# Optimization experiments

Hardware: AMD Instinct MI355X
Metric: run time of the kernel (lower is better)

The kernel has to match this reference:

```python
import jax, jax.numpy as jnp
import numpy as np

N_HEADS = 16
D_EMBED = 1024
D_CROSS = 768
D_HEAD = D_EMBED // N_HEADS
B, S = 4, 2048


def setup_inputs() -> dict:
    key = jax.random.key(0)
    ks = jax.random.split(key, 10)
    sq = lambda k, shp, fan: jax.random.normal(k, shp, jnp.float32) / np.sqrt(fan)
    return {
        "x": jax.random.normal(ks[0], (B, S, D_EMBED), jnp.float32),
        "y": jax.random.normal(ks[1], (B, S, D_CROSS), jnp.float32),
        "Wq": sq(ks[2], (D_EMBED, D_EMBED), D_EMBED),
        "bq": jnp.zeros((D_EMBED,), jnp.float32),
        "Wk": sq(ks[3], (D_CROSS, D_EMBED), D_CROSS),
        "bk": jnp.zeros((D_EMBED,), jnp.float32),
        "Wv": sq(ks[4], (D_CROSS, D_EMBED), D_CROSS),
        "bv": jnp.zeros((D_EMBED,), jnp.float32),
        "Wo": sq(ks[5], (D_EMBED, D_EMBED), D_EMBED),
        "bo": jnp.zeros((D_EMBED,), jnp.float32),
    }


def reference(x, y, Wq, bq, Wk, bk, Wv, bv, Wo, bo):
    b, s, _ = y.shape
    q = x @ Wq + bq  # [b, s, d_embed]
    k = y @ Wk + bk
    v = y @ Wv + bv
    # [b, h, s, d_head]
    q = q.reshape(b, s, N_HEADS, D_HEAD).transpose(0, 2, 1, 3)
    k = k.reshape(b, s, N_HEADS, D_HEAD).transpose(0, 2, 1, 3)
    v = v.reshape(b, s, N_HEADS, D_HEAD).transpose(0, 2, 1, 3)
    scale = 1.0 / np.sqrt(D_HEAD).astype(np.float32)
    scores = jnp.einsum("bhqd,bhkd->bhqk", q, k) * scale
    weights = jax.nn.softmax(scores, axis=-1)
    out = jnp.einsum("bhqk,bhkd->bhqd", weights, v)
    out = out.transpose(0, 2, 1, 3).reshape(x.shape)
    return out @ Wo + bo
```

## Files before the change

### kernel.cpp

```cpp
#include <hip/hip_runtime.h>

#define NHEADS 16
#define DEMBED 1024
#define DCROSS 768
#define DHEAD  64
#define BATCH  4
#define SLEN   2048
#define MROWS  (BATCH * SLEN)

using bf16   = __bf16;
using bf16x8 = __attribute__((ext_vector_type(8))) __bf16;
using bf16x4 = __attribute__((ext_vector_type(4))) __bf16;
using f32x4  = __attribute__((ext_vector_type(4))) float;

__device__ __forceinline__ f32x4 mfma_bf16(bf16x8 a, bf16x8 b, f32x4 c) {
    return __builtin_amdgcn_mfma_f32_16x16x32_bf16(a, b, c, 0, 0, 0);
}

__device__ __forceinline__ void gl2lds16(const void* g, void* l) {
    __builtin_amdgcn_global_load_lds(
        (const __attribute__((address_space(1))) void*)g,
        (__attribute__((address_space(3))) void*)l, 16, 0, 0);
}

struct PrepArgs {
    const float* wsrc[4]; bf16* wdst[4]; int wK[4];
    const float *x, *y; bf16 *xb, *yb;
};
#define NTRB 4096
__global__ void prep_all(PrepArgs a) {
    const int bid = blockIdx.x;
    const int tid = threadIdx.x;
    if (bid < NTRB) {
        __shared__ float tile[32][33];
        const int which = bid >> 10, rem = bid & 1023;
        const int K = a.wK[which], N = DEMBED;
        const int n0 = (rem & 31) * 32, k0 = (rem >> 5) * 32;
        if (k0 >= K) return;
        const float* W = a.wsrc[which];
        bf16* Wt = a.wdst[which];
        const int tx = tid & 31, ty = tid >> 5;
#pragma unroll
        for (int i = 0; i < 32; i += 8)
            tile[ty + i][tx] = W[(size_t)(k0 + ty + i) * N + n0 + tx];
        __syncthreads();
#pragma unroll
        for (int i = 0; i < 32; i += 8)
            Wt[(size_t)(n0 + ty + i) * K + k0 + tx] = (bf16)tile[tx][ty + i];
    } else {
        const int n4x = MROWS * DEMBED / 4;
        const int n4y = MROWS * DCROSS / 4;
        int i = (bid - NTRB) * 256 + tid;
        const float* src; bf16* dst; int j;
        if (i < n4x) { src = a.x; dst = a.xb; j = i; }
        else { j = i - n4x; if (j >= n4y) return; src = a.y; dst = a.yb; }
        float4 v = ((const float4*)src)[j];
        bf16x4 o = { (bf16)v.x, (bf16)v.y, (bf16)v.z, (bf16)v.w };
        ((bf16x4*)dst)[j] = o;
    }
}

struct QkvArgs {
    const bf16 *xb, *yb, *Wqt, *Wkt, *Wvt;
    const float *bq, *bk, *bv;
    bf16 *Qb, *Kb, *Vt;
    float qscale;
};
__global__ __launch_bounds__(256, 3) void gemm_qkv(QkvArgs a) {
    __shared__ bf16 As[128 * 64];
    __shared__ bf16 Bs[128 * 64];
    const int id = blockIdx.x;
    const int cls = id >> 9;
    const bf16 *A, *Bt;
    const float* bias;
    int K, m0, n0;
    if (cls == 0) { int t = id;        m0 = (t >> 3) * 128; n0 = (t & 7) * 128;
                    A = a.xb;  Bt = a.Wqt; bias = a.bq; K = DEMBED; }
    else if (cls == 1) { int t = id - 512;  m0 = (t >> 3) * 128; n0 = (t & 7) * 128;
                    A = a.yb;  Bt = a.Wkt; bias = a.bk; K = DCROSS; }
    else { int t = id - 1024; m0 = (t >> 6) * 128; n0 = (t & 63) * 128;
                    A = a.Wvt; Bt = a.yb;  bias = a.bv; K = DCROSS; }

    const int tid  = threadIdx.x;
    const int wave = tid >> 6, lane = tid & 63;
    const int quad = lane >> 4, l15 = lane & 15;
    const int wr = wave >> 1, wc = wave & 1;

    const int srow = wave * 8 + (lane >> 3);
    const int scol = ((lane & 7) ^ (lane >> 3)) * 8;
    char* ldsA0 = (char*)As + wave * 1024;
    char* ldsB0 = (char*)Bs + wave * 1024;
    const bf16* gA0 = A + (size_t)(m0 + srow) * K + scol;
    const bf16* gB0 = Bt + (size_t)(n0 + srow) * K + scol;

    const int sw = l15 & 7;

    f32x4 acc[4][4] = {};

    for (int kt = 0; kt < K; kt += 64) {
        __syncthreads();
#pragma unroll
        for (int c = 0; c < 4; c++)
            gl2lds16(gA0 + (size_t)c * 32 * K + kt, ldsA0 + c * 4096);
#pragma unroll
        for (int c = 0; c < 4; c++)
            gl2lds16(gB0 + (size_t)c * 32 * K + kt, ldsB0 + c * 4096);
        __syncthreads();

#pragma unroll
        for (int kg = 0; kg < 2; kg++) {
            bf16x8 af[4], bfr[4];
#pragma unroll
            for (int i = 0; i < 4; i++)
                af[i] = *(const bf16x8*)((const char*)As +
                         (wr * 64 + i * 16 + l15) * 128 + (((kg * 4 + quad) ^ sw) * 16));
#pragma unroll
            for (int i = 0; i < 4; i++)
                bfr[i] = *(const bf16x8*)((const char*)Bs +
                         (wc * 64 + i * 16 + l15) * 128 + (((kg * 4 + quad) ^ sw) * 16));
#pragma unroll
            for (int fr = 0; fr < 4; fr++)
#pragma unroll
                for (int fc = 0; fc < 4; fc++)
                    acc[fr][fc] = mfma_bf16(af[fr], bfr[fc], acc[fr][fc]);
        }
    }

    if (cls < 2) {
        bf16* Cout = (cls == 0) ? a.Qb : a.Kb;
        const float alpha = (cls == 0) ? a.qscale : 1.0f;
#pragma unroll
        for (int fr = 0; fr < 4; fr++) {
            int row = m0 + wr * 64 + fr * 16 + quad * 4;
#pragma unroll
            for (int fc = 0; fc < 4; fc++) {
                int col = n0 + wc * 64 + fc * 16 + l15;
                float bv = bias[col];
#pragma unroll
                for (int r = 0; r < 4; r++)
                    Cout[(size_t)(row + r) * DEMBED + col] =
                        (bf16)((acc[fr][fc][r] + bv) * alpha);
            }
        }
    } else {
        const int b = n0 >> 11;
        const size_t bbase = (size_t)b * DEMBED * SLEN;
#pragma unroll
        for (int fr = 0; fr < 4; fr++) {
            int row = m0 + wr * 64 + fr * 16 + quad * 4;
#pragma unroll
            for (int fc = 0; fc < 4; fc++) {
                int col = n0 + wc * 64 + fc * 16 + l15;
                int s = col & (SLEN - 1);
#pragma unroll
                for (int r = 0; r < 4; r++)
                    a.Vt[bbase + (size_t)(row + r) * SLEN + s] =
                        (bf16)(acc[fr][fc][r] + bias[row + r]);
            }
        }
    }
}

__global__ __launch_bounds__(256, 3) void gemm_o(const bf16* __restrict__ A,
                                                 const bf16* __restrict__ Bt,
                                                 const float* __restrict__ bias,
                                                 float* __restrict__ Cout) {
    const int K = DEMBED, N = DEMBED;
    __shared__ bf16 As[128 * 64];
    __shared__ bf16 Bs[128 * 64];
    const int tid  = threadIdx.x;
    const int wave = tid >> 6, lane = tid & 63;
    const int quad = lane >> 4, l15 = lane & 15;
    const int m0 = blockIdx.x * 128, n0 = blockIdx.y * 128;
    const int wr = wave >> 1, wc = wave & 1;

    const int srow = wave * 8 + (lane >> 3);
    const int scol = ((lane & 7) ^ (lane >> 3)) * 8;
    char* ldsA0 = (char*)As + wave * 1024;
    char* ldsB0 = (char*)Bs + wave * 1024;
    const bf16* gA0 = A + (size_t)(m0 + srow) * K + scol;
    const bf16* gB0 = Bt + (size_t)(n0 + srow) * K + scol;

    const int sw = l15 & 7;

    f32x4 acc[4][4] = {};

    for (int kt = 0; kt < K; kt += 64) {
        __syncthreads();
#pragma unroll
        for (int c = 0; c < 4; c++)
            gl2lds16(gA0 + (size_t)c * 32 * K + kt, ldsA0 + c * 4096);
#pragma unroll
        for (int c = 0; c < 4; c++)
            gl2lds16(gB0 + (size_t)c * 32 * K + kt, ldsB0 + c * 4096);
        __syncthreads();

#pragma unroll
        for (int kg = 0; kg < 2; kg++) {
            bf16x8 af[4], bfr[4];
#pragma unroll
            for (int i = 0; i < 4; i++)
                af[i] = *(const bf16x8*)((const char*)As +
                         (wr * 64 + i * 16 + l15) * 128 + (((kg * 4 + quad) ^ sw) * 16));
#pragma unroll
            for (int i = 0; i < 4; i++)
                bfr[i] = *(const bf16x8*)((const char*)Bs +
                         (wc * 64 + i * 16 + l15) * 128 + (((kg * 4 + quad) ^ sw) * 16));
#pragma unroll
            for (int fr = 0; fr < 4; fr++)
#pragma unroll
                for (int fc = 0; fc < 4; fc++)
                    acc[fr][fc] = mfma_bf16(af[fr], bfr[fc], acc[fr][fc]);
        }
    }

#pragma unroll
    for (int fr = 0; fr < 4; fr++) {
        int row = m0 + wr * 64 + fr * 16 + quad * 4;
#pragma unroll
        for (int fc = 0; fc < 4; fc++) {
            int col = n0 + wc * 64 + fc * 16 + l15;
            float bv = bias[col];
#pragma unroll
            for (int r = 0; r < 4; r++)
                Cout[(size_t)(row + r) * N + col] = acc[fr][fc][r] + bv;
        }
    }
}

__global__ __launch_bounds__(256, 4) void attn(const bf16* __restrict__ Q,
                                               const bf16* __restrict__ K,
                                               const bf16* __restrict__ Vt,
                                               bf16* __restrict__ O) {
    __shared__ bf16 KsA[64 * 64];
    __shared__ bf16 VsA[64 * 64];
    __shared__ bf16 PsA[4 * 32 * 72];

    const int tid  = threadIdx.x;
    const int wave = tid >> 6, lane = tid & 63;
    const int quad = lane >> 4, l15 = lane & 15;
    const int bh = blockIdx.x, b = bh >> 4, h = bh & 15;
    const size_t rowbase = (size_t)b * SLEN;
    const int qb = blockIdx.y * 128 + wave * 32;
    const int hc = h * DHEAD;

    bf16x8 qf[2][2];
#pragma unroll
    for (int rg = 0; rg < 2; rg++)
#pragma unroll
        for (int kg = 0; kg < 2; kg++)
            qf[rg][kg] = *(const bf16x8*)(Q + (rowbase + qb + rg * 16 + l15) * DEMBED
                                          + hc + kg * 32 + quad * 8);

    f32x4 o[2][4] = {};
    f32x4 lsv[2] = {};

    const bf16* Kbase = K + rowbase * DEMBED + hc;
    const bf16* Vbase = Vt + (size_t)bh * DHEAD * SLEN;

    const int xcol = (((tid & 7) ^ ((tid >> 3) & 7)) * 8);
    const bf16* gK = Kbase + (size_t)(tid >> 3) * DEMBED + xcol;
    const bf16* gV = Vbase + (size_t)(tid >> 3) * SLEN + xcol;
    char* ldsK = (char*)KsA + wave * 1024;
    char* ldsV = (char*)VsA + wave * 1024;
    bf16* Pw = PsA + wave * (32 * 72);

    for (int kb = 0; kb < SLEN; kb += 64) {
        __syncthreads();
        gl2lds16(gK + (size_t)kb * DEMBED, ldsK);
        gl2lds16(gK + (size_t)(kb + 32) * DEMBED, ldsK + 32 * 128);
        gl2lds16(gV + kb, ldsV);
        gl2lds16(gV + 32 * SLEN + kb, ldsV + 32 * 128);
        __syncthreads();

        f32x4 s[2][4] = {};
#pragma unroll
        for (int cg = 0; cg < 4; cg++)
#pragma unroll
            for (int kg = 0; kg < 2; kg++) {
                bf16x8 kf = *(const bf16x8*)((const char*)KsA +
                            (cg * 16 + l15) * 128 + (((kg * 4 + quad) ^ (l15 & 7)) * 16));
#pragma unroll
                for (int rg = 0; rg < 2; rg++)
                    s[rg][cg] = mfma_bf16(kf, qf[rg][kg], s[rg][cg]);
            }

#pragma unroll
        for (int rg = 0; rg < 2; rg++)
#pragma unroll
            for (int cg = 0; cg < 4; cg++) {
                f32x4 p;
                p[0] = __builtin_amdgcn_exp2f(s[rg][cg][0]);
                p[1] = __builtin_amdgcn_exp2f(s[rg][cg][1]);
                p[2] = __builtin_amdgcn_exp2f(s[rg][cg][2]);
                p[3] = __builtin_amdgcn_exp2f(s[rg][cg][3]);
                lsv[rg] += p;
                bf16x4 pb = { (bf16)p[0], (bf16)p[1], (bf16)p[2], (bf16)p[3] };
                *(bf16x4*)(Pw + (rg * 16 + l15) * 72 + cg * 16 + quad * 4) = pb;
            }

#pragma unroll
        for (int dg = 0; dg < 4; dg++)
#pragma unroll
            for (int kg = 0; kg < 2; kg++) {
                bf16x8 vf = *(const bf16x8*)((const char*)VsA +
                            (dg * 16 + l15) * 128 + (((kg * 4 + quad) ^ (l15 & 7)) * 16));
#pragma unroll
                for (int rg = 0; rg < 2; rg++)
                    o[rg][dg] = mfma_bf16(
                        *(const bf16x8*)(Pw + (rg * 16 + l15) * 72 + kg * 32 + quad * 8),
                        vf, o[rg][dg]);
            }
    }

    float inv[2];
#pragma unroll
    for (int rg = 0; rg < 2; rg++) {
        float rs = lsv[rg][0] + lsv[rg][1] + lsv[rg][2] + lsv[rg][3];
        rs += __shfl_xor(rs, 16);
        rs += __shfl_xor(rs, 32);
        inv[rg] = 1.0f / rs;
    }
#pragma unroll
    for (int rg = 0; rg < 2; rg++)
#pragma unroll
        for (int r = 0; r < 4; r++) {
            float iv = __shfl(inv[rg], quad * 4 + r);
#pragma unroll
            for (int dg = 0; dg < 4; dg++)
                O[(rowbase + qb + rg * 16 + quad * 4 + r) * DEMBED + hc + dg * 16 + l15] =
                    (bf16)(o[rg][dg][r] * iv);
        }
}

extern "C" void kernel_launch(void* const* d_in, const int* in_sizes, int n_in,
                              void* d_out, int out_size, void* d_ws, size_t ws_size,
                              hipStream_t stream) {
    const float* x  = (const float*)d_in[0];
    const float* y  = (const float*)d_in[1];
    const float* Wq = (const float*)d_in[2];
    const float* bq = (const float*)d_in[3];
    const float* Wk = (const float*)d_in[4];
    const float* bk = (const float*)d_in[5];
    const float* Wv = (const float*)d_in[6];
    const float* bv = (const float*)d_in[7];
    const float* Wo = (const float*)d_in[8];
    const float* bo = (const float*)d_in[9];
    float* out = (float*)d_out;

    char* ws = (char*)d_ws;
    size_t off = 0;
    auto alloc = [&](size_t bytes) {
        void* p = ws + off;
        off += (bytes + 255) & ~(size_t)255;
        return p;
    };
    bf16* xb  = (bf16*)alloc((size_t)MROWS * DEMBED * 2);
    bf16* yb  = (bf16*)alloc((size_t)MROWS * DCROSS * 2);
    bf16* Wqt = (bf16*)alloc((size_t)DEMBED * DEMBED * 2);
    bf16* Wkt = (bf16*)alloc((size_t)DEMBED * DCROSS * 2);
    bf16* Wvt = (bf16*)alloc((size_t)DEMBED * DCROSS * 2);
    bf16* Wot = (bf16*)alloc((size_t)DEMBED * DEMBED * 2);
    bf16* Qb  = (bf16*)alloc((size_t)MROWS * DEMBED * 2);
    bf16* Kb  = (bf16*)alloc((size_t)MROWS * DEMBED * 2);
    bf16* Vtb = (bf16*)alloc((size_t)MROWS * DEMBED * 2);
    bf16* Ab  = (bf16*)alloc((size_t)MROWS * DEMBED * 2);
    if (off > ws_size) return;

    {
        PrepArgs a;
        a.wsrc[0] = Wq; a.wdst[0] = Wqt; a.wK[0] = DEMBED;
        a.wsrc[1] = Wk; a.wdst[1] = Wkt; a.wK[1] = DCROSS;
        a.wsrc[2] = Wv; a.wdst[2] = Wvt; a.wK[2] = DCROSS;
        a.wsrc[3] = Wo; a.wdst[3] = Wot; a.wK[3] = DEMBED;
        a.x = x; a.y = y; a.xb = xb; a.yb = yb;
        int ncvt = (MROWS * DEMBED / 4 + MROWS * DCROSS / 4 + 255) / 256;
        prep_all<<<NTRB + ncvt, 256, 0, stream>>>(a);
    }

    {
        QkvArgs a;
        a.xb = xb; a.yb = yb; a.Wqt = Wqt; a.Wkt = Wkt; a.Wvt = Wvt;
        a.bq = bq; a.bk = bk; a.bv = bv;
        a.Qb = Qb; a.Kb = Kb; a.Vt = Vtb;
        a.qscale = 0.125f * 1.4426950408889634f;
        gemm_qkv<<<1536, 256, 0, stream>>>(a);
    }

    attn<<<dim3(BATCH * NHEADS, SLEN / 128), 256, 0, stream>>>(Qb, Kb, Vtb, Ab);

    gemm_o<<<dim3(MROWS / 128, DEMBED / 128), 256, 0, stream>>>(Ab, Wot, bo, out);
}
```

Baseline: 286.4 us.

## Load K/V fragments directly from global in attention, doubling query rows per wave

The attention kernel no longer stages K and V tiles in shared memory with block-wide barriers. Each wave now loads its K and V MFMA fragments straight from global memory (relying on cache) and processes 64 query rows instead of 32, so every fragment feeds more MFMAs. The grid is halved to match and launch bounds drop to 2 blocks per CU to allow the larger register footprint. The risks are uncoalesced, redundant global/L2 traffic for K/V across waves and lower occupancy.

```diff
diff --git a/kernel.cpp b/kernel.cpp
--- a/kernel.cpp
+++ b/kernel.cpp
@@ -228,101 +228,88 @@
     }
 }
 
-__global__ __launch_bounds__(256, 4) void attn(const bf16* __restrict__ Q,
+__global__ __launch_bounds__(256, 2) void attn(const bf16* __restrict__ Q,
                                                const bf16* __restrict__ K,
                                                const bf16* __restrict__ Vt,
                                                bf16* __restrict__ O) {
-    __shared__ bf16 KsA[64 * 64];
-    __shared__ bf16 VsA[64 * 64];
-    __shared__ bf16 PsA[4 * 32 * 72];
+    __shared__ bf16 PsA[4 * 64 * 72];
 
     const int tid  = threadIdx.x;
     const int wave = tid >> 6, lane = tid & 63;
     const int quad = lane >> 4, l15 = lane & 15;
     const int bh = blockIdx.x, b = bh >> 4, h = bh & 15;
     const size_t rowbase = (size_t)b * SLEN;
-    const int qb = blockIdx.y * 128 + wave * 32;
+    const int qb = blockIdx.y * 256 + wave * 64;
     const int hc = h * DHEAD;
 
-    bf16x8 qf[2][2];
-#pragma unroll
-    for (int rg = 0; rg < 2; rg++)
+    bf16x8 qf[4][2];
+#pragma unroll
+    for (int rg = 0; rg < 4; rg++)
 #pragma unroll
         for (int kg = 0; kg < 2; kg++)
             qf[rg][kg] = *(const bf16x8*)(Q + (rowbase + qb + rg * 16 + l15) * DEMBED
                                           + hc + kg * 32 + quad * 8);
 
-    f32x4 o[2][4] = {};
-    f32x4 lsv[2] = {};
-
-    const bf16* Kbase = K + rowbase * DEMBED + hc;
-    const bf16* Vbase = Vt + (size_t)bh * DHEAD * SLEN;
-
-    const int xcol = (((tid & 7) ^ ((tid >> 3) & 7)) * 8);
-    const bf16* gK = Kbase + (size_t)(tid >> 3) * DEMBED + xcol;
-    const bf16* gV = Vbase + (size_t)(tid >> 3) * SLEN + xcol;
-    char* ldsK = (char*)KsA + wave * 1024;
-    char* ldsV = (char*)VsA + wave * 1024;
-    bf16* Pw = PsA + wave * (32 * 72);
+    f32x4 o[4][4] = {};
+    f32x4 lsv[4] = {};
+
+    const bf16* Kp = K + (rowbase + l15) * DEMBED + hc + quad * 8;
+    const bf16* Vp = Vt + ((size_t)bh * DHEAD + l15) * SLEN + quad * 8;
+
+    bf16* Pw = PsA + wave * (64 * 72);
 
     for (int kb = 0; kb < SLEN; kb += 64) {
-        __syncthreads();
-        gl2lds16(gK + (size_t)kb * DEMBED, ldsK);
-        gl2lds16(gK + (size_t)(kb + 32) * DEMBED, ldsK + 32 * 128);
-        gl2lds16(gV + kb, ldsV);
-        gl2lds16(gV + 32 * SLEN + kb, ldsV + 32 * 128);
-        __syncthreads();
-
-        f32x4 s[2][4] = {};
-#pragma unroll
-        for (int cg = 0; cg < 4; cg++)
-#pragma unroll
-            for (int kg = 0; kg < 2; kg++) {
-                bf16x8 kf = *(const bf16x8*)((const char*)KsA +
-                            (cg * 16 + l15) * 128 + (((kg * 4 + quad) ^ (l15 & 7)) * 16));
-#pragma unroll
-                for (int rg = 0; rg < 2; rg++)
-                    s[rg][cg] = mfma_bf16(kf, qf[rg][kg], s[rg][cg]);
-            }
-
-#pragma unroll
-        for (int rg = 0; rg < 2; rg++)
-#pragma unroll
-            for (int cg = 0; cg < 4; cg++) {
+#pragma unroll
+        for (int cg = 0; cg < 4; cg++) {
+            const bf16* kp = Kp + (size_t)(kb + cg * 16) * DEMBED;
+            bf16x8 kf0 = *(const bf16x8*)(kp);
+            bf16x8 kf1 = *(const bf16x8*)(kp + 32);
+            f32x4 s[4] = {};
+#pragma unroll
+            for (int rg = 0; rg < 4; rg++) {
+                s[rg] = mfma_bf16(kf0, qf[rg][0], s[rg]);
+                s[rg] = mfma_bf16(kf1, qf[rg][1], s[rg]);
+            }
+#pragma unroll
+            for (int rg = 0; rg < 4; rg++) {
                 f32x4 p;
-                p[0] = __builtin_amdgcn_exp2f(s[rg][cg][0]);
-                p[1] = __builtin_amdgcn_exp2f(s[rg][cg][1]);
-                p[2] = __builtin_amdgcn_exp2f(s[rg][cg][2]);
-                p[3] = __builtin_amdgcn_exp2f(s[rg][cg][3]);
+                p[0] = __builtin_amdgcn_exp2f(s[rg][0]);
+                p[1] = __builtin_amdgcn_exp2f(s[rg][1]);
+                p[2] = __builtin_amdgcn_exp2f(s[rg][2]);
+                p[3] = __builtin_amdgcn_exp2f(s[rg][3]);
                 lsv[rg] += p;
                 bf16x4 pb = { (bf16)p[0], (bf16)p[1], (bf16)p[2], (bf16)p[3] };
                 *(bf16x4*)(Pw + (rg * 16 + l15) * 72 + cg * 16 + quad * 4) = pb;
             }
-
-#pragma unroll
-        for (int dg = 0; dg < 4; dg++)
-#pragma unroll
-            for (int kg = 0; kg < 2; kg++) {
-                bf16x8 vf = *(const bf16x8*)((const char*)VsA +
-                            (dg * 16 + l15) * 128 + (((kg * 4 + quad) ^ (l15 & 7)) * 16));
-#pragma unroll
-                for (int rg = 0; rg < 2; rg++)
-                    o[rg][dg] = mfma_bf16(
-                        *(const bf16x8*)(Pw + (rg * 16 + l15) * 72 + kg * 32 + quad * 8),
-                        vf, o[rg][dg]);
-            }
-    }
-
-    float inv[2];
-#pragma unroll
-    for (int rg = 0; rg < 2; rg++) {
+        }
+
+#pragma unroll
+        for (int dg = 0; dg < 4; dg++) {
+            const bf16* vp = Vp + (size_t)dg * 16 * SLEN + kb;
+            bf16x8 vf0 = *(const bf16x8*)(vp);
+            bf16x8 vf1 = *(const bf16x8*)(vp + 32);
+#pragma unroll
+            for (int rg = 0; rg < 4; rg++) {
+                o[rg][dg] = mfma_bf16(
+                    *(const bf16x8*)(Pw + (rg * 16 + l15) * 72 + quad * 8),
+                    vf0, o[rg][dg]);
+                o[rg][dg] = mfma_bf16(
+                    *(const bf16x8*)(Pw + (rg * 16 + l15) * 72 + 32 + quad * 8),
+                    vf1, o[rg][dg]);
+            }
+        }
+    }
+
+    float inv[4];
+#pragma unroll
+    for (int rg = 0; rg < 4; rg++) {
         float rs = lsv[rg][0] + lsv[rg][1] + lsv[rg][2] + lsv[rg][3];
         rs += __shfl_xor(rs, 16);
         rs += __shfl_xor(rs, 32);
         inv[rg] = 1.0f / rs;
     }
 #pragma unroll
-    for (int rg = 0; rg < 2; rg++)
+    for (int rg = 0; rg < 4; rg++)
 #pragma unroll
         for (int r = 0; r < 4; r++) {
             float iv = __shfl(inv[rg], quad * 4 + r);
@@ -387,7 +374,7 @@
         gemm_qkv<<<1536, 256, 0, stream>>>(a);
     }
 
-    attn<<<dim3(BATCH * NHEADS, SLEN / 128), 256, 0, stream>>>(Qb, Kb, Vtb, Ab);
+    attn<<<dim3(BATCH * NHEADS, SLEN / 256), 256, 0, stream>>>(Qb, Kb, Vtb, Ab);
 
     gemm_o<<<dim3(MROWS / 128, DEMBED / 128), 256, 0, stream>>>(Ab, Wot, bo, out);
 }
```

Result: slower. 322.0 us (+12.4%).
